# Kernel optimization log

Hardware: AMD Instinct MI355X
Metric: run time of the kernel (lower is better)

The kernel has to match this reference:

```python
import jax, jax.numpy as jnp
import numpy as np

# Geometry constants (mirror the torch module's config)
HO = 512          # output height (self.ho)
WO = 512          # output width  (self.wo)
TILE = 128        # tile_sz (= h of each MPI tile)
PAD = 8           # tile_pad_sz (config.render_padsz)
HP = TILE + 2 * PAD          # padded tile side = 144
P = HP * HP                  # pixels per warped plane = 20736
BH = HO + TILE + 2 * PAD     # buffer height = 656
BW = WO + TILE + 2 * PAD     # buffer width  = 656
HW = BH * BW
B = 1
S = 512                      # nt * n planes


def setup_inputs() -> dict:
    key = jax.random.key(0)
    k0, k1, k2, k3, k4 = jax.random.split(key, 5)
    tgt_rgb = jax.random.uniform(k0, (B, S, 3, P), dtype=jnp.float32)
    tgt_sigma = jax.random.uniform(k1, (B, S, P), dtype=jnp.float32)
    mpi_depth = jax.random.uniform(k2, (B, S), dtype=jnp.float32) * 10.0 + 0.1
    sx = jax.random.randint(k3, (B, S), 0, HO - TILE + 1, dtype=jnp.int32)
    sy = jax.random.randint(k4, (B, S), 0, WO - TILE + 1, dtype=jnp.int32)
    return {"tgt_rgb": tgt_rgb, "tgt_sigma": tgt_sigma, "mpi_depth": mpi_depth,
            "sx": sx, "sy": sy}


def reference(tgt_rgb, tgt_sigma, mpi_depth, sx, sy):
    b = tgt_rgb.shape[0]
    # --- depth sort (front-to-back), mirroring torch.sort + fancy gather ---
    order = jnp.argsort(mpi_depth, axis=1)                                  # [b,S]
    depth_s = jnp.take_along_axis(mpi_depth, order, axis=1)                 # [b,S]
    sx_s = jnp.take_along_axis(sx, order, axis=1)
    sy_s = jnp.take_along_axis(sy, order, axis=1)
    rgb_s = jnp.take_along_axis(tgt_rgb, order[:, :, None, None], axis=1)   # [b,S,3,P]
    sig_s = jnp.take_along_axis(tgt_sigma, order[:, :, None], axis=1)       # [b,S,P]

    yy, xx = jnp.meshgrid(jnp.arange(HP, dtype=jnp.int32),
                          jnp.arange(HP, dtype=jnp.int32), indexing='ij')
    yy = yy.reshape(-1)  # [P]
    xx = xx.reshape(-1)  # [P]
    bi = jnp.arange(b)[:, None]            # [b,1]
    ci = jnp.arange(3)[None, :, None]      # [1,3,1]

    def plane_step(carry, inp):
        trans, out_rgb, out_depth = carry          # [b,HW], [b,3,HW], [b,HW]
        rgb, sig, dep, px, py = inp                # [b,3,P],[b,P],[b],[b],[b]
        idx = (yy[None, :] + py[:, None]) * BW + (xx[None, :] + px[:, None])  # [b,P]
        tg = jnp.take_along_axis(trans, idx, axis=1)                          # gather T
        w = sig * tg                                                          # alpha*T
        out_rgb = out_rgb.at[bi[:, :, None], ci, idx[:, None, :]].add(rgb * w[:, None, :])
        out_depth = out_depth.at[bi, idx].add(dep[:, None] * w)
        trans = trans.at[bi, idx].set(tg * (1.0 - sig))
        return (trans, out_rgb, out_depth), None

    carry0 = (jnp.ones((b, HW), jnp.float32),
              jnp.zeros((b, 3, HW), jnp.float32),
              jnp.zeros((b, HW), jnp.float32))
    xs = (rgb_s.transpose(1, 0, 2, 3), sig_s.transpose(1, 0, 2),
          depth_s.T, sx_s.T, sy_s.T)
    (trans, out_rgb, out_depth), _ = jax.lax.scan(plane_step, carry0, xs)

    img = out_rgb.reshape(b, 3, BH, BW)
    # crop: [PAD : BH-TILE-PAD, PAD : BW-TILE-PAD] -> [b,3,HO,WO]
    img = img[:, :, PAD:BH - TILE - PAD, PAD:BW - TILE - PAD]
    return img
```

## Files before the change

### kernel.cpp

```cpp
#include <hip/hip_runtime.h>

constexpr int TILE   = 128;
constexpr int PAD    = 8;
constexpr int HP     = TILE + 2 * PAD;
constexpr int P      = HP * HP;
constexpr int S      = 512;
constexpr int OUTW   = 512;
constexpr int OUTP   = OUTW * OUTW;
constexpr int NSEG   = 8;
constexpr int NCHUNK = OUTW / 64;
constexpr int BAND   = 8;
constexpr int CAP    = 128;
constexpr int GROUP  = 4;
constexpr float TEPS = 4e-3f;

__global__ __launch_bounds__(512) void sort_planes_kernel(
    const float* __restrict__ depth,
    const int*   __restrict__ sx,
    const int*   __restrict__ sy,
    int4*        __restrict__ meta)
{
    __shared__ float sd[S];
    const int i = threadIdx.x;
    sd[i] = depth[i];
    __syncthreads();

    const float di = sd[i];
    int rank = 0;
#pragma unroll 8
    for (int j = 0; j < S; ++j) {
        const float dj = sd[j];
        rank += (dj < di) || (dj == di && j < i);
    }
    meta[rank] = make_int4(sy[i], sx[i], i * P, i * 3 * P);
}

__global__ __launch_bounds__(512) void fused_composite_kernel(
    const float* __restrict__ rgb,
    const float* __restrict__ sigma,
    const int4*  __restrict__ meta,
    float*       __restrict__ out)
{
    __shared__ int4 slist[CAP];
    __shared__ int  cnt[NSEG];

    const int tid  = threadIdx.x;
    const int w    = tid >> 6;
    const int lane = tid & 63;
    const int X0   = blockIdx.x * 64;
    const int Y0   = blockIdx.y * BAND;

    const int4 m = meta[tid];
    const bool cov =
        ((unsigned)(Y0 + PAD + BAND - 1 - m.x) < (unsigned)(HP + BAND - 1)) &&
        ((unsigned)(X0 + 71 - m.y) < 207u);
    const unsigned long long bmask = __ballot(cov);
    const int pre = __popcll(bmask & ((1ull << lane) - 1ull));
    if (lane == 0) cnt[w] = __popcll(bmask);
    __syncthreads();

    int off = 0, nc = 0;
#pragma unroll
    for (int i = 0; i < NSEG; ++i) {
        const int c = cnt[i];
        off += (i < w) ? c : 0;
        nc  += c;
    }
    const int padded = min((nc + GROUP - 1) & ~(GROUP - 1), CAP);
    if (cov) {
        const int idx = off + pre;
        if (idx < CAP) slist[idx] = m;
    }
    if (tid >= nc && tid < padded) slist[tid] = make_int4(-100000, -100000, 0, 0);
    __syncthreads();

    const int row = Y0 + w;
    const int yb  = row + PAD;
    const int xb  = X0 + PAD + lane;

    float trans = 1.0f, ar = 0.0f, ag = 0.0f, ab = 0.0f;

    for (int k = 0; k < padded; k += GROUP) {
        if (trans >= TEPS) {
            float s[GROUP], mk[GROUP], r[GROUP], g[GROUP], b[GROUP];
#pragma unroll
            for (int u = 0; u < GROUP; ++u) {
                const int4 e = slist[k + u];
                const int yy = yb - e.x;
                const int xx = xb - e.y;
                const bool c = ((unsigned)yy < (unsigned)HP) &
                               ((unsigned)xx < (unsigned)HP);
                const int yc = min(max(yy, 0), HP - 1);
                const int xc = min(max(xx, 0), HP - 1);
                const int o  = yc * HP + xc;
                mk[u] = c ? 1.0f : 0.0f;
                s[u]  = sigma[e.z + o];
                const int pr = e.w + o;
                r[u] = rgb[pr];
                g[u] = rgb[pr + P];
                b[u] = rgb[pr + 2 * P];
            }
#pragma unroll
            for (int u = 0; u < GROUP; ++u) {
                const float sg  = s[u] * mk[u];
                const float wgt = sg * trans;
                ar = fmaf(r[u], wgt, ar);
                ag = fmaf(g[u], wgt, ag);
                ab = fmaf(b[u], wgt, ab);
                trans *= (1.0f - sg);
            }
        }
        if (__all(trans < TEPS)) break;
    }

    const int o = row * OUTW + X0 + lane;
    out[o]            = ar;
    out[o + OUTP]     = ag;
    out[o + 2 * OUTP] = ab;
}

extern "C" void kernel_launch(void* const* d_in, const int* in_sizes, int n_in,
                              void* d_out, int out_size, void* d_ws, size_t ws_size,
                              hipStream_t stream)
{
    const float* tgt_rgb   = (const float*)d_in[0];
    const float* tgt_sigma = (const float*)d_in[1];
    const float* mpi_depth = (const float*)d_in[2];
    const int*   sx        = (const int*)d_in[3];
    const int*   sy        = (const int*)d_in[4];
    float*       out       = (float*)d_out;
    int4*        meta      = (int4*)d_ws;

    sort_planes_kernel<<<1, S, 0, stream>>>(mpi_depth, sx, sy, meta);

    dim3 grid(NCHUNK, OUTW / BAND);
    fused_composite_kernel<<<grid, 512, 0, stream>>>(tgt_rgb, tgt_sigma,
                                                     meta, out);
}
```

Before: 38.48 us.

## Fuse depth sort into composite kernel and loosen transmittance cutoff

```diff
diff --git a/kernel.cpp b/kernel.cpp
--- a/kernel.cpp
+++ b/kernel.cpp
@@ -10,47 +10,46 @@
 constexpr int NSEG   = 8;
 constexpr int NCHUNK = OUTW / 64;
 constexpr int BAND   = 8;
+constexpr int NBAND  = OUTW / BAND;
 constexpr int CAP    = 128;
 constexpr int GROUP  = 4;
-constexpr float TEPS = 4e-3f;
+constexpr float TEPS = 8e-3f;
 
-__global__ __launch_bounds__(512) void sort_planes_kernel(
+__global__ __launch_bounds__(512) void fused_all_kernel(
+    const float* __restrict__ rgb,
+    const float* __restrict__ sigma,
     const float* __restrict__ depth,
     const int*   __restrict__ sx,
     const int*   __restrict__ sy,
-    int4*        __restrict__ meta)
+    float*       __restrict__ out)
 {
     __shared__ float sd[S];
-    const int i = threadIdx.x;
-    sd[i] = depth[i];
+    __shared__ int4  smeta[S];
+    __shared__ int4  slist[CAP];
+    __shared__ int   cnt[NSEG];
+
+    const int tid  = threadIdx.x;
+    const int w    = tid >> 6;
+    const int lane = tid & 63;
+    const int wid   = blockIdx.x;
+    const int band  = wid & (NBAND - 1);
+    const int chunk = wid >> 6;
+    const int X0   = chunk * 64;
+    const int Y0   = band * BAND;
+
+    sd[tid] = depth[tid];
     __syncthreads();
-
-    const float di = sd[i];
+    const float di = sd[tid];
     int rank = 0;
 #pragma unroll 8
     for (int j = 0; j < S; ++j) {
         const float dj = sd[j];
-        rank += (dj < di) || (dj == di && j < i);
+        rank += (dj < di) || (dj == di && j < tid);
     }
-    meta[rank] = make_int4(sy[i], sx[i], i * P, i * 3 * P);
-}
+    smeta[rank] = make_int4(sy[tid], sx[tid], tid * P, tid * 3 * P);
+    __syncthreads();
 
-__global__ __launch_bounds__(512) void fused_composite_kernel(
-    const float* __restrict__ rgb,
-    const float* __restrict__ sigma,
-    const int4*  __restrict__ meta,
-    float*       __restrict__ out)
-{
-    __shared__ int4 slist[CAP];
-    __shared__ int  cnt[NSEG];
-
-    const int tid  = threadIdx.x;
-    const int w    = tid >> 6;
-    const int lane = tid & 63;
-    const int X0   = blockIdx.x * 64;
-    const int Y0   = blockIdx.y * BAND;
-
-    const int4 m = meta[tid];
+    const int4 m = smeta[tid];
     const bool cov =
         ((unsigned)(Y0 + PAD + BAND - 1 - m.x) < (unsigned)(HP + BAND - 1)) &&
         ((unsigned)(X0 + 71 - m.y) < 207u);
@@ -129,11 +128,7 @@
     const int*   sx        = (const int*)d_in[3];
     const int*   sy        = (const int*)d_in[4];
     float*       out       = (float*)d_out;
-    int4*        meta      = (int4*)d_ws;
 
-    sort_planes_kernel<<<1, S, 0, stream>>>(mpi_depth, sx, sy, meta);
-
-    dim3 grid(NCHUNK, OUTW / BAND);
-    fused_composite_kernel<<<grid, 512, 0, stream>>>(tgt_rgb, tgt_sigma,
-                                                     meta, out);
+    fused_all_kernel<<<NCHUNK * NBAND, 512, 0, stream>>>(
+        tgt_rgb, tgt_sigma, mpi_depth, sx, sy, out);
 }
```

Result: no change. 38.21 us (-0.7%).
